# Kernel optimization log

Measured on AMD Instinct MI355X. Metric: run time of the kernel, lower is better.

Reference implementation:

```python
import jax, jax.numpy as jnp
import numpy as np

EMBED = 1024
HEADS = 16
HEAD_DIM = EMBED // HEADS
FF = 4096
B, T = 2, 2048


def setup_inputs() -> dict:
    key = jax.random.key(0)
    ks = jax.random.split(key, 12)
    s = lambda k, shape, fan: jax.random.normal(k, shape, jnp.float32) * (1.0 / np.sqrt(fan))
    return {
        "x": jax.random.normal(ks[0], (B, T, EMBED), jnp.float32),
        "qkv_w": s(ks[1], (EMBED, 3 * EMBED), EMBED),
        "qkv_b": jnp.zeros((3 * EMBED,), jnp.float32),
        "out_w": s(ks[2], (EMBED, EMBED), EMBED),
        "out_b": jnp.zeros((EMBED,), jnp.float32),
        "ff_w1": s(ks[3], (EMBED, FF), EMBED),
        "ff_b1": jnp.zeros((FF,), jnp.float32),
        "ff_w2": s(ks[4], (FF, EMBED), FF),
        "ff_b2": jnp.zeros((EMBED,), jnp.float32),
        "ln1_g": jnp.ones((EMBED,), jnp.float32),
        "ln1_b": jnp.zeros((EMBED,), jnp.float32),
        "ln2_g": jnp.ones((EMBED,), jnp.float32),
        "ln2_b": jnp.zeros((EMBED,), jnp.float32),
    }


def _layer_norm(x, g, b, eps=1e-5):
    mu = jnp.mean(x, axis=-1, keepdims=True)
    var = jnp.var(x, axis=-1, keepdims=True)
    return (x - mu) * jax.lax.rsqrt(var + eps) * g + b


def _attention(x, qkv_w, qkv_b, out_w, out_b):
    Bv, Tv, C = x.shape
    qkv = x @ qkv_w + qkv_b                      # [B,T,3C]
    qkv = qkv.reshape(Bv, Tv, 3, HEADS, HEAD_DIM)
    q, k, v = qkv[:, :, 0], qkv[:, :, 1], qkv[:, :, 2]  # [B,T,H,D]
    scale = 1.0 / np.sqrt(HEAD_DIM)
    scores = jnp.einsum("bqhd,bkhd->bhqk", q, k) * scale  # [B,H,T,T]
    attn = jax.nn.softmax(scores, axis=-1)
    out = jnp.einsum("bhqk,bkhd->bqhd", attn, v).reshape(Bv, Tv, C)
    return out @ out_w + out_b


def _ffn(x, w1, b1, w2, b2):
    h = jax.nn.gelu(x @ w1 + b1, approximate=False)
    return h @ w2 + b2


def reference(x, qkv_w, qkv_b, out_w, out_b, ff_w1, ff_b1, ff_w2, ff_b2,
              ln1_g, ln1_b, ln2_g, ln2_b):
    x = x + _attention(_layer_norm(x, ln1_g, ln1_b), qkv_w, qkv_b, out_w, out_b)
    x = x + _ffn(_layer_norm(x, ln2_g, ln2_b), ff_w1, ff_b1, ff_w2, ff_b2)
    return x
```

## Files before the change

### kernel.cpp

```cpp
#include <hip/hip_runtime.h>

#define E     1024
#define HEADS 16
#define HD    64
#define FFD   4096
#define TT    2048
#define MMDIM 4096
#define NKV   1024
#define PO    (32 * 2048 * 64)

typedef __bf16 bf16x8 __attribute__((ext_vector_type(8)));
typedef float f32x4 __attribute__((ext_vector_type(4)));
typedef float f32x16 __attribute__((ext_vector_type(16)));
typedef unsigned short u16;
typedef unsigned u32;
typedef u16 ushort8 __attribute__((ext_vector_type(8)));
typedef u16 us4 __attribute__((ext_vector_type(4)));
typedef u32 u32x4 __attribute__((ext_vector_type(4)));

__device__ __forceinline__ u16 f2bf(float f) {
  unsigned u = __float_as_uint(f);
  u = (u + 0x7fffu + ((u >> 16) & 1u)) >> 16;
  return (u16)u;
}
__device__ __forceinline__ float bf2f(u16 u) {
  return __uint_as_float(((unsigned)u) << 16);
}
__device__ __forceinline__ u32 cvtpk(float a, float b) {
  u32 r;
  asm("v_cvt_pk_bf16_f32 %0, %1, %2" : "=v"(r) : "v"(a), "v"(b));
  return r;
}

__device__ __forceinline__ void gload_lds16(const void* g, void* l) {
  __builtin_amdgcn_global_load_lds((__attribute__((address_space(1))) void*)g,
                                   (__attribute__((address_space(3))) void*)l,
                                   16, 0, 0);
}

__global__ void __launch_bounds__(256) ln_kernel(const float* __restrict__ x,
                                                 const float* __restrict__ g,
                                                 const float* __restrict__ b,
                                                 u16* __restrict__ out) {
  int row = blockIdx.x;
  int t = threadIdx.x;
  const float4 v = reinterpret_cast<const float4*>(x + (size_t)row * E)[t];
  float s = v.x + v.y + v.z + v.w;
  float s2 = v.x * v.x + v.y * v.y + v.z * v.z + v.w * v.w;
#pragma unroll
  for (int m = 1; m < 64; m <<= 1) {
    s += __shfl_xor(s, m);
    s2 += __shfl_xor(s2, m);
  }
  __shared__ float red[8];
  int wave = t >> 6, lane = t & 63;
  if (lane == 0) { red[wave] = s; red[wave + 4] = s2; }
  __syncthreads();
  s = red[0] + red[1] + red[2] + red[3];
  s2 = red[4] + red[5] + red[6] + red[7];
  float mean = s * (1.f / E);
  float var = s2 * (1.f / E) - mean * mean;
  float inv = rsqrtf(var + 1e-5f);
  const float4 gv = reinterpret_cast<const float4*>(g)[t];
  const float4 bv = reinterpret_cast<const float4*>(b)[t];
  us4 pk;
  pk.x = f2bf((v.x - mean) * inv * gv.x + bv.x);
  pk.y = f2bf((v.y - mean) * inv * gv.y + bv.y);
  pk.z = f2bf((v.z - mean) * inv * gv.z + bv.z);
  pk.w = f2bf((v.w - mean) * inv * gv.w + bv.w);
  *(us4*)(out + (size_t)row * E + t * 4) = pk;
}

__global__ void __launch_bounds__(256) transpose_bf16(const float* __restrict__ in,
                                                      u16* __restrict__ out,
                                                      int K, int N) {
  __shared__ float tile[32][33];
  int k0 = blockIdx.y * 32, n0 = blockIdx.x * 32;
  int tx = threadIdx.x, ty = threadIdx.y;
#pragma unroll
  for (int i = ty; i < 32; i += 8)
    tile[i][tx] = in[(size_t)(k0 + i) * N + n0 + tx];
  __syncthreads();
#pragma unroll
  for (int i = ty; i < 32; i += 8)
    out[(size_t)(n0 + i) * K + k0 + tx] = f2bf(tile[tx][i]);
}

template <int MODE>
__global__ void __launch_bounds__(256) gemm4b(const u16* __restrict__ Aa,
                                              const u16* __restrict__ Bt,
                                              const float* __restrict__ bias,
                                              const float* __restrict__ resid,
                                              u16* __restrict__ ob0,
                                              u16* __restrict__ ob1,
                                              u16* __restrict__ ob2,
                                              float* __restrict__ of,
                                              int N, int K, int lda, int ldb) {
  __shared__ __align__(16) u16 As[4][128 * 32];
  __shared__ __align__(16) u16 Bs[4][128 * 32];
  const int n0 = blockIdx.x * 128, m0 = blockIdx.y * 128;
  const int tid = threadIdx.x, lane = tid & 63;
  const int wave = tid >> 6, wr = wave >> 1, wc = wave & 1;
  const int l15 = lane & 15, hi4 = lane >> 4;
  const size_t koff = (size_t)blockIdx.z * K;
  const int nt = K >> 5;

  f32x4 acc[4][4];
#pragma unroll
  for (int i = 0; i < 4; i++)
#pragma unroll
    for (int j = 0; j < 4; j++) acc[i][j] = (f32x4){0.f, 0.f, 0.f, 0.f};

  const u16* ApR[2];
  const u16* BpR[2];
  int cst[2];
#pragma unroll
  for (int r = 0; r < 2; r++) {
    int c = tid + r * 256;
    int row = c >> 2, ch = c & 3;
    cst[r] = c;
    ApR[r] = Aa + (size_t)(m0 + row) * lda + koff + ch * 8;
    BpR[r] = Bt + (size_t)(n0 + row) * ldb + koff + ch * 8;
  }

#define STAGE4B(T)                                                             \
  do {                                                                         \
    int buf_ = (T) & 3;                                                        \
    int k0_ = (T) << 5;                                                        \
    _Pragma("unroll") for (int r_ = 0; r_ < 2; r_++) {                         \
      gload_lds16(ApR[r_] + k0_, (char*)&As[buf_][0] + cst[r_] * 16);          \
      gload_lds16(BpR[r_] + k0_, (char*)&Bs[buf_][0] + cst[r_] * 16);          \
    }                                                                          \
  } while (0)

  STAGE4B(0);
  STAGE4B(1);
  asm volatile("s_waitcnt vmcnt(4)" ::: "memory");
  __builtin_amdgcn_s_barrier();
  __builtin_amdgcn_sched_barrier(0);

  for (int t = 0; t < nt; ++t) {
    if (t + 2 < nt) STAGE4B(t + 2);
    const char* ab = (const char*)&As[t & 3][0];
    const char* bb = (const char*)&Bs[t & 3][0];
    bf16x8 a[4], b[4];
#pragma unroll
    for (int i = 0; i < 4; i++)
      a[i] = *(const bf16x8*)(ab + (wr * 64 + i * 16 + l15) * 64 + hi4 * 16);
#pragma unroll
    for (int j = 0; j < 4; j++)
      b[j] = *(const bf16x8*)(bb + (wc * 64 + j * 16 + l15) * 64 + hi4 * 16);
    asm volatile("s_waitcnt lgkmcnt(0)" ::: "memory");
    __builtin_amdgcn_sched_barrier(0);
    __builtin_amdgcn_s_setprio(1);
#pragma unroll
    for (int i = 0; i < 4; i++)
#pragma unroll
      for (int j = 0; j < 4; j++)
        acc[i][j] = __builtin_amdgcn_mfma_f32_16x16x32_bf16(a[i], b[j], acc[i][j], 0, 0, 0);
    __builtin_amdgcn_s_setprio(0);
    asm volatile("s_waitcnt vmcnt(4)" ::: "memory");
    __builtin_amdgcn_s_barrier();
    __builtin_amdgcn_sched_barrier(0);
  }
#undef STAGE4B

#pragma unroll
  for (int i = 0; i < 4; i++) {
#pragma unroll
    for (int j = 0; j < 4; j++) {
      int mb = m0 + wr * 64 + i * 16 + (hi4 << 2);
      int n = n0 + wc * 64 + j * 16 + l15;
      float bv = (MODE == 3) ? 0.f : bias[n];
      float v4[4];
#pragma unroll
      for (int r = 0; r < 4; r++) v4[r] = acc[i][j][r] + bv;
      if (MODE == 0) {
        int b_ = mb >> 11;
        int t = mb & 2047;
        int s = n >> 10;
        int hd = n & 1023;
        int h_ = hd >> 6;
        int d = hd & 63;
        size_t bh = (size_t)b_ * HEADS + h_;
        if (s == 0) {
#pragma unroll
          for (int r = 0; r < 4; r++)
            ob0[(bh * TT + (t + r)) * HD + d] = f2bf(v4[r] * 0.125f);
        } else if (s == 1) {
#pragma unroll
          for (int r = 0; r < 4; r++)
            ob1[(bh * TT + (t + r)) * HD + d] = f2bf(v4[r]);
        } else {
          us4 pk;
#pragma unroll
          for (int r = 0; r < 4; r++) pk[r] = f2bf(v4[r]);
          *(us4*)&ob2[(bh * HD + d) * TT + t] = pk;
        }
      } else if (MODE == 1) {
#pragma unroll
        for (int r = 0; r < 4; r++) {
          size_t idx = (size_t)(mb + r) * E + n;
          of[idx] = v4[r] + resid[idx];
        }
      } else if (MODE == 2) {
#pragma unroll
        for (int r = 0; r < 4; r++)
          ob0[(size_t)(mb + r) * FFD + n] =
              f2bf(0.5f * v4[r] * (1.f + erff(v4[r] * 0.70710678118f)));
      } else {
        if (blockIdx.z == 0) {
          float bz = bias[n];
#pragma unroll
          for (int r = 0; r < 4; r++) {
            size_t idx = (size_t)(mb + r) * E + n;
            of[idx] = v4[r] + bz + resid[idx];
          }
        } else {
#pragma unroll
          for (int r = 0; r < 4; r++)
            ob0[(size_t)(mb + r) * N + n] = f2bf(v4[r]);
        }
      }
    }
  }
}

__global__ void __launch_bounds__(256) ff2_reduce(const u16* __restrict__ p1,
                                                  float* __restrict__ out) {
  size_t i = ((size_t)blockIdx.x * 256 + threadIdx.x) * 4;
  us4 a = *(const us4*)(p1 + i);
  float4 o = *(const float4*)(out + i);
  o.x += bf2f(a.x);
  o.y += bf2f(a.y);
  o.z += bf2f(a.z);
  o.w += bf2f(a.w);
  *(float4*)(out + i) = o;
}

__global__ void __launch_bounds__(512, 4) attn_kernel(const u16* __restrict__ Qb,
                                                      const u16* __restrict__ Kb,
                                                      const u16* __restrict__ Vt,
                                                      u16* __restrict__ op,
                                                      float2* __restrict__ ml) {
  __shared__ __align__(16) u16 Ks[2][64 * 64];
  __shared__ __align__(16) u16 Vs[2][64 * 64];
  const int bid = blockIdx.x;
  const int bh = bid & 31;
  const int qblk = (bid >> 5) & 7;
  const int part = bid >> 8;
  const int pstart = part * NKV;
  const int tid = threadIdx.x;
  const int w = tid >> 6, lane = tid & 63;
  const int lq = lane & 31, hi = lane >> 5;
  const int q0 = qblk * 256 + w * 32;

  const u16* Qp = Qb + ((size_t)bh * TT + q0 + lq) * HD + hi * 8;
  bf16x8 qf[4];
#pragma unroll
  for (int c = 0; c < 4; c++) qf[c] = *(const bf16x8*)(Qp + c * 16);

  const int srow = tid >> 3, schk = tid & 7;
  const u16* Kg = Kb + ((size_t)bh * TT + pstart + srow) * HD + ((schk ^ (srow & 7)) * 8);
  const u16* Vg = Vt + ((size_t)bh * HD + srow) * TT + pstart + ((schk ^ (srow & 7)) * 8);
  u16* kdst = &Ks[0][0] + tid * 8;
  u16* vdst = &Vs[0][0] + tid * 8;

  int ofs[8];
#pragma unroll
  for (int c = 0; c < 8; c++) ofs[c] = (c ^ (lq & 7)) << 4;

  f32x16 o0, o1;
#pragma unroll
  for (int r = 0; r < 16; r++) { o0[r] = 0.f; o1[r] = 0.f; }
  float m_run = -1e30f, l_run = 0.f;

#define STAGEKV(T, BUF)                                                        \
  do {                                                                         \
    gload_lds16(Kg + (size_t)(T) * 64 * HD, kdst + (BUF) * 4096);              \
    gload_lds16(Vg + (T) * 64, vdst + (BUF) * 4096);                           \
  } while (0)

  STAGEKV(0, 0);
  asm volatile("s_waitcnt vmcnt(0)" ::: "memory");
  __builtin_amdgcn_s_barrier();
  __builtin_amdgcn_sched_barrier(0);

  const int NT = NKV / 64;
  for (int t = 0; t < NT; ++t) {
    const int buf = t & 1;
    if (t + 1 < NT) STAGEKV(t + 1, buf ^ 1);
    const char* kT = (const char*)&Ks[buf][0];
    const char* vT = (const char*)&Vs[buf][0];
#pragma unroll
    for (int ss = 0; ss < 2; ++ss) {
      const char* kR = kT + (ss * 32 + lq) * 128;
      bf16x8 kf[4];
#pragma unroll
      for (int c = 0; c < 4; c++) kf[c] = *(const bf16x8*)(kR + ofs[c * 2 + hi]);
      const char* vR0 = vT + lq * 128;
      const char* vR1 = vT + (32 + lq) * 128;
      bf16x8 v00 = *(const bf16x8*)(vR0 + ofs[ss * 4 + 0 + hi]);
      bf16x8 v01 = *(const bf16x8*)(vR0 + ofs[ss * 4 + 2 + hi]);
      bf16x8 v10 = *(const bf16x8*)(vR1 + ofs[ss * 4 + 0 + hi]);
      bf16x8 v11 = *(const bf16x8*)(vR1 + ofs[ss * 4 + 2 + hi]);
      asm volatile("s_waitcnt lgkmcnt(0)" ::: "memory");
      __builtin_amdgcn_sched_barrier(0);

      f32x16 s;
#pragma unroll
      for (int r = 0; r < 16; r++) s[r] = 0.f;
      __builtin_amdgcn_s_setprio(1);
#pragma unroll
      for (int c = 0; c < 4; c++)
        s = __builtin_amdgcn_mfma_f32_32x32x16_bf16(kf[c], qf[c], s, 0, 0, 0);
      __builtin_amdgcn_s_setprio(0);

      float mx = s[0];
#pragma unroll
      for (int r = 1; r < 16; r++) mx = fmaxf(mx, s[r]);
      mx = fmaxf(mx, __shfl_xor(mx, 32));

      if (__any(mx > m_run + 8.f)) {
        float mn = fmaxf(m_run, mx);
        float al = __expf(m_run - mn);
#pragma unroll
        for (int r = 0; r < 16; r++) { o0[r] *= al; o1[r] *= al; }
        l_run *= al;
        m_run = mn;
      }

      float p[16], ps = 0.f;
#pragma unroll
      for (int r = 0; r < 16; r++) {
        p[r] = __expf(s[r] - m_run);
        ps += p[r];
      }
      l_run += ps + __shfl_xor(ps, 32);

      u32 wv[8];
#pragma unroll
      for (int c = 0; c < 2; c++) {
        u32 qA = cvtpk(p[c * 8 + 0], p[c * 8 + 1]);
        u32 qB = cvtpk(p[c * 8 + 2], p[c * 8 + 3]);
        u32 qC = cvtpk(p[c * 8 + 4], p[c * 8 + 5]);
        u32 qD = cvtpk(p[c * 8 + 6], p[c * 8 + 7]);
        u32 As_ = __shfl_xor(qA, 32), Bs_ = __shfl_xor(qB, 32);
        u32 Cs_ = __shfl_xor(qC, 32), Ds_ = __shfl_xor(qD, 32);
        wv[c * 4 + 0] = hi ? Cs_ : qA;
        wv[c * 4 + 1] = hi ? Ds_ : qB;
        wv[c * 4 + 2] = hi ? qC : As_;
        wv[c * 4 + 3] = hi ? qD : Bs_;
      }
      u32x4 t0 = {wv[0], wv[1], wv[2], wv[3]};
      u32x4 t1 = {wv[4], wv[5], wv[6], wv[7]};
      bf16x8 pf0 = __builtin_bit_cast(bf16x8, t0);
      bf16x8 pf1 = __builtin_bit_cast(bf16x8, t1);

      __builtin_amdgcn_s_setprio(1);
      o0 = __builtin_amdgcn_mfma_f32_32x32x16_bf16(v00, pf0, o0, 0, 0, 0);
      o0 = __builtin_amdgcn_mfma_f32_32x32x16_bf16(v01, pf1, o0, 0, 0, 0);
      o1 = __builtin_amdgcn_mfma_f32_32x32x16_bf16(v10, pf0, o1, 0, 0, 0);
      o1 = __builtin_amdgcn_mfma_f32_32x32x16_bf16(v11, pf1, o1, 0, 0, 0);
      __builtin_amdgcn_s_setprio(0);
    }
    asm volatile("s_waitcnt vmcnt(0)" ::: "memory");
    __builtin_amdgcn_s_barrier();
    __builtin_amdgcn_sched_barrier(0);
  }
#undef STAGEKV

  float rl = 1.f / l_run;
  u16* opP = op + (size_t)part * PO + ((size_t)bh * TT + q0 + lq) * HD;
#pragma unroll
  for (int r = 0; r < 16; r++) {
    int d = (r & 3) + ((r >> 2) << 3) + (hi << 2);
    opP[d] = f2bf(o0[r] * rl);
    opP[32 + d] = f2bf(o1[r] * rl);
  }
  if (hi == 0) {
    float2 v;
    v.x = m_run;
    v.y = l_run;
    ml[(size_t)part * (32 * TT) + bh * TT + q0 + lq] = v;
  }
}

__global__ void __launch_bounds__(256) attn_merge(const u16* __restrict__ op,
                                                  const float2* __restrict__ ml,
                                                  u16* __restrict__ O) {
  int idx = blockIdx.x * 256 + threadIdx.x;
  int bh = idx >> 14;
  int q = (idx >> 3) & 2047;
  int d0 = (idx & 7) * 8;
  int mli = bh * TT + q;
  float2 ab0 = ml[mli];
  float2 ab1 = ml[32 * TT + mli];
  float ms = fmaxf(ab0.x, ab1.x);
  float w0 = ab0.y * __expf(ab0.x - ms);
  float w1 = ab1.y * __expf(ab1.x - ms);
  float inv = 1.f / (w0 + w1);
  w0 *= inv;
  w1 *= inv;
  size_t base = ((size_t)bh * TT + q) * HD + d0;
  ushort8 a = *(const ushort8*)(op + base);
  ushort8 b = *(const ushort8*)(op + PO + base);
  ushort8 o;
#pragma unroll
  for (int k = 0; k < 8; k++) o[k] = f2bf(w0 * bf2f(a[k]) + w1 * bf2f(b[k]));
  size_t obase = ((size_t)(bh >> 4) * TT + q) * E + (bh & 15) * HD + d0;
  *(ushort8*)(O + obase) = o;
}

extern "C" void kernel_launch(void* const* d_in, const int* in_sizes, int n_in,
                              void* d_out, int out_size, void* d_ws, size_t ws_size,
                              hipStream_t stream) {
  (void)in_sizes; (void)n_in; (void)out_size; (void)ws_size;
  const float* x = (const float*)d_in[0];
  const float* qkv_w = (const float*)d_in[1];
  const float* qkv_b = (const float*)d_in[2];
  const float* out_w = (const float*)d_in[3];
  const float* out_b = (const float*)d_in[4];
  const float* ff_w1 = (const float*)d_in[5];
  const float* ff_b1 = (const float*)d_in[6];
  const float* ff_w2 = (const float*)d_in[7];
  const float* ff_b2 = (const float*)d_in[8];
  const float* ln1_g = (const float*)d_in[9];
  const float* ln1_b = (const float*)d_in[10];
  const float* ln2_g = (const float*)d_in[11];
  const float* ln2_b = (const float*)d_in[12];

  char* ws = (char*)d_ws;
  u16* outwt = (u16*)(ws + 0);
  u16* ffw1t = (u16*)(ws + 2097152);
  u16* ffw2t = (u16*)(ws + 10485760);
  u16* qkvwt = (u16*)(ws + 18874368);
  u16* ln_out = (u16*)(ws + 25165824);
  float* x1 = (float*)(ws + 33554432);
  u16* qb = (u16*)(ws + 50331648);
  u16* kb = (u16*)(ws + 58720256);
  u16* vt = (u16*)(ws + 67108864);
  u16* attn_o = (u16*)(ws + 75497472);
  u16* opbuf = (u16*)(ws + 18874368);
  float2* mlbuf = (float2*)(ws + 35651584);
  u16* hbuf = (u16*)(ws + 50331648);
  u16* pbuf = (u16*)(ws + 0);

  dim3 tb(32, 8);
  transpose_bf16<<<dim3(3072 / 32, 1024 / 32), tb, 0, stream>>>(qkv_w, qkvwt, 1024, 3072);
  transpose_bf16<<<dim3(1024 / 32, 1024 / 32), tb, 0, stream>>>(out_w, outwt, 1024, 1024);
  transpose_bf16<<<dim3(4096 / 32, 1024 / 32), tb, 0, stream>>>(ff_w1, ffw1t, 1024, 4096);
  transpose_bf16<<<dim3(1024 / 32, 4096 / 32), tb, 0, stream>>>(ff_w2, ffw2t, 4096, 1024);

  ln_kernel<<<MMDIM, 256, 0, stream>>>(x, ln1_g, ln1_b, ln_out);
  gemm4b<0><<<dim3(3072 / 128, MMDIM / 128), 256, 0, stream>>>(
      ln_out, qkvwt, qkv_b, nullptr, qb, kb, vt, nullptr, 3072, 1024, 1024, 1024);
  attn_kernel<<<dim3(2 * 8 * 32), 512, 0, stream>>>(qb, kb, vt, opbuf, mlbuf);
  attn_merge<<<dim3(32 * TT * 8 / 256), 256, 0, stream>>>(opbuf, mlbuf, attn_o);
  gemm4b<1><<<dim3(1024 / 128, MMDIM / 128), 256, 0, stream>>>(
      attn_o, outwt, out_b, x, nullptr, nullptr, nullptr, x1, 1024, 1024, 1024, 1024);
  ln_kernel<<<MMDIM, 256, 0, stream>>>(x1, ln2_g, ln2_b, ln_out);
  gemm4b<2><<<dim3(4096 / 128, MMDIM / 128), 256, 0, stream>>>(
      ln_out, ffw1t, ff_b1, nullptr, hbuf, nullptr, nullptr, nullptr, 4096, 1024, 1024, 1024);
  gemm4b<3><<<dim3(1024 / 128, MMDIM / 128, 2), 256, 0, stream>>>(
      hbuf, ffw2t, ff_b2, x1, pbuf, nullptr, nullptr, (float*)d_out, 1024, 2048, 4096, 4096);
  ff2_reduce<<<(size_t)MMDIM * E / 1024, 256, 0, stream>>>(pbuf, (float*)d_out);
}
```

Measured before the change: 298.1 us.

## Replace 128x128 GEMM with 256x256 eight-wave tile and 4-way split-K

Replaces the 128x128, 4-wave GEMM with a 256x256 tile run by 8 waves. It uses 128KB of dynamic LDS, XOR-swizzled shared-memory layout and a phased double-buffered pipeline with K-step 64. The out-projection and FF2 GEMMs now use 4-way split-K, with partials written in bf16 to scattered workspace regions and summed by a new three-input reduce kernel. This targets better data reuse and more work per CU on the 256-CU part, but it adds partial-sum traffic, bf16 rounding of partials, grids of only 192–256 blocks, and complicated workspace aliasing.

Measured after the change: 350.2 us. 17.5% more time.

```diff
diff --git a/kernel.cpp b/kernel.cpp
--- a/kernel.cpp
+++ b/kernel.cpp
@@ -87,94 +87,108 @@
 }
 
 template <int MODE>
-__global__ void __launch_bounds__(256) gemm4b(const u16* __restrict__ Aa,
-                                              const u16* __restrict__ Bt,
-                                              const float* __restrict__ bias,
-                                              const float* __restrict__ resid,
-                                              u16* __restrict__ ob0,
-                                              u16* __restrict__ ob1,
-                                              u16* __restrict__ ob2,
-                                              float* __restrict__ of,
-                                              int N, int K, int lda, int ldb) {
-  __shared__ __align__(16) u16 As[4][128 * 32];
-  __shared__ __align__(16) u16 Bs[4][128 * 32];
-  const int n0 = blockIdx.x * 128, m0 = blockIdx.y * 128;
+__global__ void __launch_bounds__(512, 2)
+gemm8p(const u16* __restrict__ Aa, const u16* __restrict__ Bt,
+       const float* __restrict__ bias, const float* __restrict__ resid,
+       u16* __restrict__ ob0, u16* __restrict__ ob1, u16* __restrict__ ob2,
+       float* __restrict__ of,
+       u16* __restrict__ p1a, u16* __restrict__ p1b,
+       u16* __restrict__ p2a, u16* __restrict__ p2b,
+       u16* __restrict__ p3a, u16* __restrict__ p3b,
+       int N, int K, int lda, int ldb) {
+  extern __shared__ char lds[];
+  const int n0 = blockIdx.x * 256, m0 = blockIdx.y * 256;
   const int tid = threadIdx.x, lane = tid & 63;
-  const int wave = tid >> 6, wr = wave >> 1, wc = wave & 1;
+  const int w = tid >> 6, wr = w >> 2, wc = w & 3;
   const int l15 = lane & 15, hi4 = lane >> 4;
   const size_t koff = (size_t)blockIdx.z * K;
-  const int nt = K >> 5;
-
-  f32x4 acc[4][4];
-#pragma unroll
-  for (int i = 0; i < 4; i++)
+  const int nt = K >> 6;
+
+  f32x4 acc[8][4];
+#pragma unroll
+  for (int i = 0; i < 8; i++)
 #pragma unroll
     for (int j = 0; j < 4; j++) acc[i][j] = (f32x4){0.f, 0.f, 0.f, 0.f};
 
-  const u16* ApR[2];
-  const u16* BpR[2];
-  int cst[2];
-#pragma unroll
-  for (int r = 0; r < 2; r++) {
-    int c = tid + r * 256;
-    int row = c >> 2, ch = c & 3;
-    cst[r] = c;
-    ApR[r] = Aa + (size_t)(m0 + row) * lda + koff + ch * 8;
-    BpR[r] = Bt + (size_t)(n0 + row) * ldb + koff + ch * 8;
-  }
-
-#define STAGE4B(T)                                                             \
+  const int srow = tid >> 2;
+  const int slog = (((tid & 3) ^ ((tid >> 2) & 3) ^ ((tid >> 4) & 3))) * 8;
+  const u16* Ast0 = Aa + (size_t)(m0 + srow) * lda + koff + slog;
+  const u16* Bst0 = Bt + (size_t)(n0 + srow) * ldb + koff + slog;
+  const size_t arst = (size_t)128 * lda, brst = (size_t)128 * ldb;
+
+  const int rdoff = ((hi4 ^ (l15 & 3) ^ ((l15 >> 2) & 3)) << 4);
+
+#define STG(T, MAT, KH)                                                        \
   do {                                                                         \
-    int buf_ = (T) & 3;                                                        \
-    int k0_ = (T) << 5;                                                        \
-    _Pragma("unroll") for (int r_ = 0; r_ < 2; r_++) {                         \
-      gload_lds16(ApR[r_] + k0_, (char*)&As[buf_][0] + cst[r_] * 16);          \
-      gload_lds16(BpR[r_] + k0_, (char*)&Bs[buf_][0] + cst[r_] * 16);          \
+    int tc_ = (T) < nt ? (T) : nt - 1;                                         \
+    char* d_ = lds + (((T) & 1) << 16) + ((MAT) << 15) + ((KH) << 14) + tid * 16; \
+    if (MAT == 0) {                                                            \
+      const u16* g_ = Ast0 + tc_ * 64 + (KH) * 32;                             \
+      gload_lds16(g_, d_);                                                     \
+      gload_lds16(g_ + arst, d_ + 8192);                                       \
+    } else {                                                                   \
+      const u16* g_ = Bst0 + tc_ * 64 + (KH) * 32;                             \
+      gload_lds16(g_, d_);                                                     \
+      gload_lds16(g_ + brst, d_ + 8192);                                       \
     }                                                                          \
   } while (0)
 
-  STAGE4B(0);
-  STAGE4B(1);
-  asm volatile("s_waitcnt vmcnt(4)" ::: "memory");
+#define PHASE(MF0, KH, BUF, RDB, ST, SM, SK, DOVM)                             \
+  do {                                                                         \
+    const char* ab_ = lds + ((BUF) << 16) + ((KH) << 14);                      \
+    _Pragma("unroll") for (int q_ = 0; q_ < 4; q_++)                           \
+      a[q_] = *(const bf16x8*)(ab_ + (wr * 128 + ((MF0) + q_) * 16 + l15) * 64 + rdoff); \
+    if (RDB) {                                                                 \
+      const char* bb_ = lds + ((BUF) << 16) + 32768 + ((KH) << 14);            \
+      _Pragma("unroll") for (int q_ = 0; q_ < 4; q_++)                         \
+        b[q_] = *(const bf16x8*)(bb_ + (wc * 64 + q_ * 16 + l15) * 64 + rdoff); \
+    }                                                                          \
+    STG(ST, SM, SK);                                                           \
+    asm volatile("s_waitcnt lgkmcnt(0)" ::: "memory");                         \
+    __builtin_amdgcn_sched_barrier(0);                                         \
+    __builtin_amdgcn_s_setprio(1);                                             \
+    _Pragma("unroll") for (int mi_ = 0; mi_ < 4; mi_++)                        \
+      _Pragma("unroll") for (int nj_ = 0; nj_ < 4; nj_++)                      \
+        acc[(MF0) + mi_][nj_] = __builtin_amdgcn_mfma_f32_16x16x32_bf16(       \
+            a[mi_], b[nj_], acc[(MF0) + mi_][nj_], 0, 0, 0);                   \
+    __builtin_amdgcn_s_setprio(0);                                             \
+    if (DOVM) asm volatile("s_waitcnt vmcnt(8)" ::: "memory");                 \
+    __builtin_amdgcn_s_barrier();                                              \
+    __builtin_amdgcn_sched_barrier(0);                                         \
+  } while (0)
+
+  STG(0, 0, 0); STG(0, 1, 0); STG(0, 0, 1); STG(0, 1, 1);
+  STG(1, 0, 0); STG(1, 1, 0);
+  asm volatile("s_waitcnt vmcnt(8)" ::: "memory");
   __builtin_amdgcn_s_barrier();
   __builtin_amdgcn_sched_barrier(0);
 
-  for (int t = 0; t < nt; ++t) {
-    if (t + 2 < nt) STAGE4B(t + 2);
-    const char* ab = (const char*)&As[t & 3][0];
-    const char* bb = (const char*)&Bs[t & 3][0];
-    bf16x8 a[4], b[4];
-#pragma unroll
-    for (int i = 0; i < 4; i++)
-      a[i] = *(const bf16x8*)(ab + (wr * 64 + i * 16 + l15) * 64 + hi4 * 16);
-#pragma unroll
-    for (int j = 0; j < 4; j++)
-      b[j] = *(const bf16x8*)(bb + (wc * 64 + j * 16 + l15) * 64 + hi4 * 16);
-    asm volatile("s_waitcnt lgkmcnt(0)" ::: "memory");
-    __builtin_amdgcn_sched_barrier(0);
-    __builtin_amdgcn_s_setprio(1);
-#pragma unroll
-    for (int i = 0; i < 4; i++)
-#pragma unroll
-      for (int j = 0; j < 4; j++)
-        acc[i][j] = __builtin_amdgcn_mfma_f32_16x16x32_bf16(a[i], b[j], acc[i][j], 0, 0, 0);
-    __builtin_amdgcn_s_setprio(0);
-    asm volatile("s_waitcnt vmcnt(4)" ::: "memory");
-    __builtin_amdgcn_s_barrier();
-    __builtin_amdgcn_sched_barrier(0);
+  bf16x8 a[4], b[4];
+  const int niter = nt >> 1;
+  for (int i = 0; i < niter; ++i) {
+    const int T0 = 2 * i;
+    PHASE(0, 0, 0, 1, T0 + 1, 0, 1, 0);
+    PHASE(4, 0, 0, 0, T0 + 1, 1, 1, 1);
+    PHASE(0, 1, 0, 1, T0 + 2, 0, 0, 0);
+    PHASE(4, 1, 0, 0, T0 + 2, 1, 0, 1);
+    PHASE(0, 0, 1, 1, T0 + 2, 0, 1, 0);
+    PHASE(4, 0, 1, 0, T0 + 2, 1, 1, 1);
+    PHASE(0, 1, 1, 1, T0 + 3, 0, 0, 0);
+    PHASE(4, 1, 1, 0, T0 + 3, 1, 0, 1);
   }
-#undef STAGE4B
-
-#pragma unroll
-  for (int i = 0; i < 4; i++) {
-#pragma unroll
-    for (int j = 0; j < 4; j++) {
-      int mb = m0 + wr * 64 + i * 16 + (hi4 << 2);
-      int n = n0 + wc * 64 + j * 16 + l15;
+#undef PHASE
+#undef STG
+
+#pragma unroll
+  for (int mi = 0; mi < 8; mi++) {
+#pragma unroll
+    for (int nj = 0; nj < 4; nj++) {
+      int mb = m0 + wr * 128 + mi * 16 + (hi4 << 2);
+      int n = n0 + wc * 64 + nj * 16 + l15;
       float bv = (MODE == 3) ? 0.f : bias[n];
       float v4[4];
 #pragma unroll
-      for (int r = 0; r < 4; r++) v4[r] = acc[i][j][r] + bv;
+      for (int r = 0; r < 4; r++) v4[r] = acc[mi][nj][r] + bv;
       if (MODE == 0) {
         int b_ = mb >> 11;
         int t = mb & 2047;
@@ -197,19 +211,14 @@
           for (int r = 0; r < 4; r++) pk[r] = f2bf(v4[r]);
           *(us4*)&ob2[(bh * HD + d) * TT + t] = pk;
         }
-      } else if (MODE == 1) {
-#pragma unroll
-        for (int r = 0; r < 4; r++) {
-          size_t idx = (size_t)(mb + r) * E + n;
-          of[idx] = v4[r] + resid[idx];
-        }
       } else if (MODE == 2) {
 #pragma unroll
         for (int r = 0; r < 4; r++)
           ob0[(size_t)(mb + r) * FFD + n] =
               f2bf(0.5f * v4[r] * (1.f + erff(v4[r] * 0.70710678118f)));
       } else {
-        if (blockIdx.z == 0) {
+        int z = blockIdx.z;
+        if (z == 0) {
           float bz = bias[n];
 #pragma unroll
           for (int r = 0; r < 4; r++) {
@@ -217,24 +226,43 @@
             of[idx] = v4[r] + bz + resid[idx];
           }
         } else {
+          u16* pa = (z == 1) ? p1a : ((z == 2) ? p2a : p3a);
+          u16* pb = (z == 1) ? p1b : ((z == 2) ? p2b : p3b);
+          u16* pz;
+          int mrow = mb;
+          if (mb < 3072) pz = pa;
+          else { pz = pb; mrow = mb - 3072; }
 #pragma unroll
           for (int r = 0; r < 4; r++)
-            ob0[(size_t)(mb + r) * N + n] = f2bf(v4[r]);
+            pz[(size_t)(mrow + r) * N + n] = f2bf(v4[r]);
         }
       }
     }
   }
 }
 
-__global__ void __launch_bounds__(256) ff2_reduce(const u16* __restrict__ p1,
-                                                  float* __restrict__ out) {
+__global__ void __launch_bounds__(256) red3(const u16* __restrict__ p1a,
+                                            const u16* __restrict__ p1b,
+                                            const u16* __restrict__ p2a,
+                                            const u16* __restrict__ p2b,
+                                            const u16* __restrict__ p3a,
+                                            const u16* __restrict__ p3b,
+                                            float* __restrict__ out) {
   size_t i = ((size_t)blockIdx.x * 256 + threadIdx.x) * 4;
-  us4 a = *(const us4*)(p1 + i);
+  int row = (int)(i >> 10);
+  bool lo = row < 3072;
+  size_t ib = i - (size_t)3072 * 1024;
+  const u16* q1 = lo ? (p1a + i) : (p1b + ib);
+  const u16* q2 = lo ? (p2a + i) : (p2b + ib);
+  const u16* q3 = lo ? (p3a + i) : (p3b + ib);
+  us4 a = *(const us4*)q1;
+  us4 b = *(const us4*)q2;
+  us4 c = *(const us4*)q3;
   float4 o = *(const float4*)(out + i);
-  o.x += bf2f(a.x);
-  o.y += bf2f(a.y);
-  o.z += bf2f(a.z);
-  o.w += bf2f(a.w);
+  o.x += bf2f(a.x) + bf2f(b.x) + bf2f(c.x);
+  o.y += bf2f(a.y) + bf2f(b.y) + bf2f(c.y);
+  o.z += bf2f(a.z) + bf2f(b.z) + bf2f(c.z);
+  o.w += bf2f(a.w) + bf2f(b.w) + bf2f(c.w);
   *(float4*)(out + i) = o;
 }
 
@@ -444,7 +472,22 @@
   u16* opbuf = (u16*)(ws + 18874368);
   float2* mlbuf = (float2*)(ws + 35651584);
   u16* hbuf = (u16*)(ws + 50331648);
-  u16* pbuf = (u16*)(ws + 0);
+  u16* prj1 = (u16*)(ws + 50331648);
+  u16* prj2 = (u16*)(ws + 58720256);
+  u16* prj3 = (u16*)(ws + 67108864);
+  u16* pf1a = (u16*)(ws + 2097152);
+  u16* pf1b = (u16*)(ws + 2097152 + (size_t)3072 * 1024 * 2);
+  u16* pf2a = (u16*)(ws + 27262976);
+  u16* pf2b = (u16*)(ws + 0);
+  u16* pf3a = (u16*)(ws + 18874368);
+  u16* pf3b = (u16*)(ws + 25165824);
+
+  hipFuncSetAttribute((const void*)gemm8p<0>,
+                      hipFuncAttributeMaxDynamicSharedMemorySize, 131072);
+  hipFuncSetAttribute((const void*)gemm8p<2>,
+                      hipFuncAttributeMaxDynamicSharedMemorySize, 131072);
+  hipFuncSetAttribute((const void*)gemm8p<3>,
+                      hipFuncAttributeMaxDynamicSharedMemorySize, 131072);
 
   dim3 tb(32, 8);
   transpose_bf16<<<dim3(3072 / 32, 1024 / 32), tb, 0, stream>>>(qkv_w, qkvwt, 1024, 3072);
@@ -453,16 +496,25 @@
   transpose_bf16<<<dim3(1024 / 32, 4096 / 32), tb, 0, stream>>>(ff_w2, ffw2t, 4096, 1024);
 
   ln_kernel<<<MMDIM, 256, 0, stream>>>(x, ln1_g, ln1_b, ln_out);
-  gemm4b<0><<<dim3(3072 / 128, MMDIM / 128), 256, 0, stream>>>(
-      ln_out, qkvwt, qkv_b, nullptr, qb, kb, vt, nullptr, 3072, 1024, 1024, 1024);
+  gemm8p<0><<<dim3(12, 16), 512, 131072, stream>>>(
+      ln_out, qkvwt, qkv_b, nullptr, qb, kb, vt, nullptr,
+      nullptr, nullptr, nullptr, nullptr, nullptr, nullptr, 3072, 1024, 1024, 1024);
   attn_kernel<<<dim3(2 * 8 * 32), 512, 0, stream>>>(qb, kb, vt, opbuf, mlbuf);
   attn_merge<<<dim3(32 * TT * 8 / 256), 256, 0, stream>>>(opbuf, mlbuf, attn_o);
-  gemm4b<1><<<dim3(1024 / 128, MMDIM / 128), 256, 0, stream>>>(
-      attn_o, outwt, out_b, x, nullptr, nullptr, nullptr, x1, 1024, 1024, 1024, 1024);
+  gemm8p<3><<<dim3(4, 16, 4), 512, 131072, stream>>>(
+      attn_o, outwt, out_b, x, nullptr, nullptr, nullptr, x1,
+      prj1, prj1 + (size_t)3072 * 1024, prj2, prj2 + (size_t)3072 * 1024,
+      prj3, prj3 + (size_t)3072 * 1024, 1024, 256, 1024, 1024);
+  red3<<<(size_t)MMDIM * E / 1024, 256, 0, stream>>>(
+      prj1, prj1 + (size_t)3072 * 1024, prj2, prj2 + (size_t)3072 * 1024,
+      prj3, prj3 + (size_t)3072 * 1024, x1);
   ln_kernel<<<MMDIM, 256, 0, stream>>>(x1, ln2_g, ln2_b, ln_out);
-  gemm4b<2><<<dim3(4096 / 128, MMDIM / 128), 256, 0, stream>>>(
-      ln_out, ffw1t, ff_b1, nullptr, hbuf, nullptr, nullptr, nullptr, 4096, 1024, 1024, 1024);
-  gemm4b<3><<<dim3(1024 / 128, MMDIM / 128, 2), 256, 0, stream>>>(
-      hbuf, ffw2t, ff_b2, x1, pbuf, nullptr, nullptr, (float*)d_out, 1024, 2048, 4096, 4096);
-  ff2_reduce<<<(size_t)MMDIM * E / 1024, 256, 0, stream>>>(pbuf, (float*)d_out);
-}
+  gemm8p<2><<<dim3(16, 16), 512, 131072, stream>>>(
+      ln_out, ffw1t, ff_b1, nullptr, hbuf, nullptr, nullptr, nullptr,
+      nullptr, nullptr, nullptr, nullptr, nullptr, nullptr, 4096, 1024, 1024, 1024);
+  gemm8p<3><<<dim3(4, 16, 4), 512, 131072, stream>>>(
+      hbuf, ffw2t, ff_b2, x1, nullptr, nullptr, nullptr, (float*)d_out,
+      pf1a, pf1b, pf2a, pf2b, pf3a, pf3b, 1024, 1024, 4096, 4096);
+  red3<<<(size_t)MMDIM * E / 1024, 256, 0, stream>>>(
+      pf1a, pf1b, pf2a, pf2b, pf3a, pf3b, (float*)d_out);
+}
```
